# Performance work log

Measured on AMD Instinct MI355X. Metric: run time of the kernel, lower is better.

## Reference

```python
import jax, jax.numpy as jnp
import numpy as np

NUM_HEADS = 16
NUM_KV_HEADS = 4
HEAD_SIZE = 128
SCALE = 1.0 / np.sqrt(128.0).astype(np.float32)
NEG_INF = -1e30


def setup_inputs() -> dict:
    key = jax.random.key(0)
    kq, kk, kv = jax.random.split(key, 3)
    B, S = 2, 2048
    query = jax.random.normal(kq, (B, NUM_HEADS, S, HEAD_SIZE), dtype=jnp.float32)
    k = jax.random.normal(kk, (B, NUM_KV_HEADS, S, HEAD_SIZE), dtype=jnp.float32)
    v = jax.random.normal(kv, (B, NUM_KV_HEADS, S, HEAD_SIZE), dtype=jnp.float32)
    return {"query": query, "key": k, "value": v}


def _attn(query, key, value):
    # query: [B, H, S, D]; key/value: [B, Hkv, S, D]; GQA with group = H // Hkv
    B, H, S, D = query.shape
    Hkv = key.shape[1]
    G = H // Hkv
    q = query.reshape(B, Hkv, G, S, D)
    # scores: [B, Hkv, G, Sq, Sk]
    scores = jnp.einsum('bkgsd,bktd->bkgst', q, key) * jnp.float32(SCALE)
    causal = jnp.tril(jnp.ones((S, S), dtype=bool))  # [Sq, Sk]
    scores = jnp.where(causal, scores, jnp.float32(NEG_INF))
    probs = jax.nn.softmax(scores, axis=-1)
    out = jnp.einsum('bkgst,bktd->bkgsd', probs, value)  # [B, Hkv, G, S, D]
    out = out.reshape(B, H, S, D)
    # transpose(1,2).reshape -> [B, S, H*D]
    return out.transpose(0, 2, 1, 3).reshape(B, S, H * D)


def reference(query, key, value):
    return _attn(query, key, value)
```

## Files before the change

### kernel.cpp

```cpp
#include <hip/hip_runtime.h>


#define S_LEN 2048
#define DH    128
#define NH    16
#define NKVH  4
#define NB    2
#define TQ    128
#define TK    64
#define NQT   (S_LEN / TQ)
#define PROW  72
#define QSCALE 0.12752749610559243f

typedef __attribute__((ext_vector_type(8))) short short8;
typedef __attribute__((ext_vector_type(4))) float f32x4;

#if __has_builtin(__builtin_amdgcn_exp2f)
#define EX2(x) __builtin_amdgcn_exp2f(x)
#else
#define EX2(x) exp2f(x)
#endif

__device__ __forceinline__ unsigned short bf1(float a) {
    union { float f; unsigned u; } x; x.f = a;
    return (unsigned short)((x.u + 0x8000u) >> 16);
}
__device__ __forceinline__ unsigned pk2(float a, float b) {
    union { float f; unsigned u; } x, y; x.f = a; y.f = b;
    return ((x.u + 0x8000u) >> 16) | ((y.u + 0x8000u) & 0xffff0000u);
}
__device__ __forceinline__ void cp16(const void* g, void* lds) {
    __builtin_amdgcn_global_load_lds(
        (const __attribute__((address_space(1))) void*)g,
        (__attribute__((address_space(3))) void*)lds, 16, 0, 0);
}

__global__ __launch_bounds__(256, 4)
void prepack(const float* __restrict__ K, const float* __restrict__ V,
             unsigned short* __restrict__ Kb, unsigned short* __restrict__ Vt) {
    const long long flat = (long long)blockIdx.x * 2048 + threadIdx.x * 8;
    const int s = (int)(flat >> 7) & (S_LEN - 1);
    const int d0 = (int)flat & 127;
    if (blockIdx.y == 0) {
        const float* p = K + flat;
        float4 x = *(const float4*)p;
        float4 y = *(const float4*)(p + 4);
        const int cs = (d0 >> 3) ^ (s & 7);
        uint4 o;
        o.x = pk2(x.x, x.y); o.y = pk2(x.z, x.w);
        o.z = pk2(y.x, y.y); o.w = pk2(y.z, y.w);
        *(uint4*)(Kb + (flat & ~127LL) + cs * 8) = o;
    } else {
        const float* p = V + flat;
        float4 x = *(const float4*)p;
        float4 y = *(const float4*)(p + 4);
        float vals[8] = {x.x, x.y, x.z, x.w, y.x, y.y, y.z, y.w};
        unsigned short* vt = Vt + ((flat >> 18) << 18);
        const int sc = (s >> 3) & 7, sbase = s & ~63, soff = s & 7;
#pragma unroll
        for (int dd = 0; dd < 8; ++dd) {
            const int d = d0 + dd;
            vt[(long long)d * S_LEN + sbase + ((sc ^ (d & 7)) << 3) + soff] = bf1(vals[dd]);
        }
    }
}

__global__ __launch_bounds__(256, 2)
void attn_fwd(const float* __restrict__ Q,
              const unsigned short* __restrict__ Kb,
              const unsigned short* __restrict__ Vtg,
              float* __restrict__ O) {
    const int qt  = NQT - 1 - blockIdx.x;
    const int h   = blockIdx.y;
    const int b   = blockIdx.z;
    const int kvh = h >> 2;

    const int tid  = threadIdx.x;
    const int w    = tid >> 6;
    const int lane = tid & 63;
    const int quad = lane >> 4;
    const int l16  = lane & 15;
    const int swz  = l16 & 7;

    __shared__ alignas(16) unsigned short Kl[TK][DH];
    __shared__ alignas(16) unsigned short Vl[DH][TK];
    __shared__ alignas(16) unsigned short Pl[TQ][PROW];

    const unsigned short* kb = Kb  + ((size_t)b * NKVH + kvh) * (size_t)(S_LEN * DH);
    const unsigned short* vb = Vtg + ((size_t)b * NKVH + kvh) * (size_t)(S_LEN * DH);

    const int wq0 = qt * TQ + w * 32;
    short8 aq[2][4];
#pragma unroll
    for (int sub = 0; sub < 2; ++sub) {
        const float* qp = Q + (((size_t)b * NH + h) * S_LEN + wq0 + sub * 16 + l16) * DH;
#pragma unroll
        for (int dc = 0; dc < 4; ++dc) {
            float4 x = *(const float4*)(qp + dc * 32 + quad * 8);
            float4 y = *(const float4*)(qp + dc * 32 + quad * 8 + 4);
            union { unsigned u[4]; short8 s; } t;
            t.u[0] = pk2(x.x * QSCALE, x.y * QSCALE);
            t.u[1] = pk2(x.z * QSCALE, x.w * QSCALE);
            t.u[2] = pk2(y.x * QSCALE, y.y * QSCALE);
            t.u[3] = pk2(y.z * QSCALE, y.w * QSCALE);
            aq[sub][dc] = t.s;
        }
    }

    f32x4 o[2][8];
#pragma unroll
    for (int sub = 0; sub < 2; ++sub)
#pragma unroll
        for (int ch = 0; ch < 8; ++ch) o[sub][ch] = (f32x4){0.f, 0.f, 0.f, 0.f};
    float lsum[2][4];
#pragma unroll
    for (int sub = 0; sub < 2; ++sub)
#pragma unroll
        for (int r = 0; r < 4; ++r) lsum[sub][r] = 0.f;

    const int nt  = 2 * qt + 2;
    const int ntw = 2 * qt + 1 + (w >> 1);

    for (int t = 0; t < nt; ++t) {
        const int j0 = t * TK;
        __syncthreads();
        {
            const char* ks = (const char*)(kb + (size_t)j0 * DH);
#pragma unroll
            for (int i = 0; i < 4; ++i)
                cp16(ks + w * 4096 + i * 1024 + lane * 16,
                     (char*)&Kl[0][0] + w * 4096 + i * 1024);
            const char* vs = (const char*)vb;
#pragma unroll
            for (int i = 0; i < 4; ++i) {
                const int row  = w * 32 + i * 8 + (lane >> 3);
                const int colB = (lane & 7) * 16;
                cp16(vs + (size_t)row * (S_LEN * 2) + j0 * 2 + colB,
                     (char*)&Vl[0][0] + w * 4096 + i * 1024);
            }
        }
        __syncthreads();

        if (t < ntw) {
            const bool diag = (t == ntw - 1);
            f32x4 s[2][4];
#pragma unroll
            for (int sub = 0; sub < 2; ++sub)
#pragma unroll
                for (int k4 = 0; k4 < 4; ++k4) s[sub][k4] = (f32x4){0.f, 0.f, 0.f, 0.f};
#pragma unroll
            for (int dc = 0; dc < 4; ++dc) {
#pragma unroll
                for (int k4 = 0; k4 < 4; ++k4) {
                    short8 bk = *(const short8*)&Kl[k4 * 16 + l16][((dc * 4 + quad) ^ swz) * 8];
                    s[0][k4] = __builtin_amdgcn_mfma_f32_16x16x32_bf16(aq[0][dc], bk, s[0][k4], 0, 0, 0);
                    s[1][k4] = __builtin_amdgcn_mfma_f32_16x16x32_bf16(aq[1][dc], bk, s[1][k4], 0, 0, 0);
                }
            }
#pragma unroll
            for (int sub = 0; sub < 2; ++sub) {
                const int rb = wq0 + sub * 16 + quad * 4;
#pragma unroll
                for (int r = 0; r < 4; ++r) {
                    float v0 = s[sub][0][r], v1 = s[sub][1][r];
                    float v2 = s[sub][2][r], v3 = s[sub][3][r];
                    if (diag) {
                        const int row = rb + r;
                        if (j0 + l16      > row) v0 = -1e30f;
                        if (j0 + 16 + l16 > row) v1 = -1e30f;
                        if (j0 + 32 + l16 > row) v2 = -1e30f;
                        if (j0 + 48 + l16 > row) v3 = -1e30f;
                    }
                    float p0 = EX2(v0), p1 = EX2(v1), p2 = EX2(v2), p3 = EX2(v3);
                    lsum[sub][r] += (p0 + p1) + (p2 + p3);
                    const int prow = w * 32 + sub * 16 + quad * 4 + r;
                    Pl[prow][l16]      = bf1(p0);
                    Pl[prow][16 + l16] = bf1(p1);
                    Pl[prow][32 + l16] = bf1(p2);
                    Pl[prow][48 + l16] = bf1(p3);
                }
            }
#pragma unroll
            for (int kc = 0; kc < 2; ++kc) {
                short8 ap0 = *(const short8*)&Pl[w * 32 + l16][kc * 32 + quad * 8];
                short8 ap1 = *(const short8*)&Pl[w * 32 + 16 + l16][kc * 32 + quad * 8];
#pragma unroll
                for (int ch = 0; ch < 8; ++ch) {
                    short8 bv = *(const short8*)&Vl[ch * 16 + l16][((kc * 4 + quad) ^ swz) * 8];
                    o[0][ch] = __builtin_amdgcn_mfma_f32_16x16x32_bf16(ap0, bv, o[0][ch], 0, 0, 0);
                    o[1][ch] = __builtin_amdgcn_mfma_f32_16x16x32_bf16(ap1, bv, o[1][ch], 0, 0, 0);
                }
            }
        }
    }

#pragma unroll
    for (int sub = 0; sub < 2; ++sub) {
#pragma unroll
        for (int r = 0; r < 4; ++r) {
            float rs = lsum[sub][r];
            rs += __shfl_xor(rs, 1);
            rs += __shfl_xor(rs, 2);
            rs += __shfl_xor(rs, 4);
            rs += __shfl_xor(rs, 8);
            const float invl = 1.f / rs;
            const int row = wq0 + sub * 16 + quad * 4 + r;
            float* op = O + ((size_t)b * S_LEN + row) * (NH * DH) + h * DH;
#pragma unroll
            for (int ch = 0; ch < 8; ++ch)
                op[ch * 16 + l16] = o[sub][ch][r] * invl;
        }
    }
}

extern "C" void kernel_launch(void* const* d_in, const int* in_sizes, int n_in,
                              void* d_out, int out_size, void* d_ws, size_t ws_size,
                              hipStream_t stream) {
    const float* Q = (const float*)d_in[0];
    const float* K = (const float*)d_in[1];
    const float* V = (const float*)d_in[2];
    float* O = (float*)d_out;
    unsigned short* Kb = (unsigned short*)d_ws;
    unsigned short* Vt = Kb + (size_t)NB * NKVH * S_LEN * DH;
    dim3 pgrid(NB * NKVH * (S_LEN / 16), 2);
    prepack<<<pgrid, 256, 0, stream>>>(K, V, Kb, Vt);
    dim3 grid(NQT, NH, NB);
    attn_fwd<<<grid, 256, 0, stream>>>(Q, Kb, Vt, O);
}
```

Before: 170.9 us.

## Transpose V through LDS in prepack, pack P stores, reorder attention grid

The V prepack now stages a 64x32 tile in shared memory and writes coalesced 16-byte rows of the transposed, swizzled layout, replacing scattered 2-byte global stores. In the attention kernel, P is written to LDS as packed 8-byte stores with a permuted key order that the V layout mirrors. The grid is flattened to 1D with batch 0 scheduled heavy-first and batch 1 light-first, to balance causal work across CUs. The mixed ordering of the two batches risks an uneven tail.

```diff
diff --git a/kernel.cpp b/kernel.cpp
--- a/kernel.cpp
+++ b/kernel.cpp
@@ -38,10 +38,10 @@
 __global__ __launch_bounds__(256, 4)
 void prepack(const float* __restrict__ K, const float* __restrict__ V,
              unsigned short* __restrict__ Kb, unsigned short* __restrict__ Vt) {
-    const long long flat = (long long)blockIdx.x * 2048 + threadIdx.x * 8;
-    const int s = (int)(flat >> 7) & (S_LEN - 1);
-    const int d0 = (int)flat & 127;
     if (blockIdx.y == 0) {
+        const long long flat = (long long)blockIdx.x * 2048 + threadIdx.x * 8;
+        const int s = (int)(flat >> 7) & (S_LEN - 1);
+        const int d0 = (int)flat & 127;
         const float* p = K + flat;
         float4 x = *(const float4*)p;
         float4 y = *(const float4*)(p + 4);
@@ -51,17 +51,37 @@
         o.z = pk2(y.x, y.y); o.w = pk2(y.z, y.w);
         *(uint4*)(Kb + (flat & ~127LL) + cs * 8) = o;
     } else {
-        const float* p = V + flat;
-        float4 x = *(const float4*)p;
-        float4 y = *(const float4*)(p + 4);
-        float vals[8] = {x.x, x.y, x.z, x.w, y.x, y.y, y.z, y.w};
-        unsigned short* vt = Vt + ((flat >> 18) << 18);
-        const int sc = (s >> 3) & 7, sbase = s & ~63, soff = s & 7;
-#pragma unroll
-        for (int dd = 0; dd < 8; ++dd) {
-            const int d = d0 + dd;
-            vt[(long long)d * S_LEN + sbase + ((sc ^ (d & 7)) << 3) + soff] = bf1(vals[dd]);
-        }
+        const int x = blockIdx.x;
+        const int bkvh = x >> 7, sblk = (x >> 2) & 31, q = x & 3;
+        const int tid = threadIdx.x;
+        __shared__ unsigned Lt[64][17];
+        const float* base = V + (size_t)bkvh * S_LEN * DH + (size_t)sblk * 64 * DH + q * 32;
+#pragma unroll
+        for (int j = 0; j < 2; ++j) {
+            const int e = tid + j * 256;
+            const int s = e >> 3, c4 = e & 7;
+            float4 v = *(const float4*)(base + (size_t)s * DH + c4 * 4);
+            Lt[s][c4 * 2]     = pk2(v.x, v.y);
+            Lt[s][c4 * 2 + 1] = pk2(v.z, v.w);
+        }
+        __syncthreads();
+        const unsigned short* lt = (const unsigned short*)&Lt[0][0];
+        const int d_loc = tid >> 3, pc = tid & 7;
+        const int d = q * 32 + d_loc;
+        const int c_log = pc ^ (d & 7);
+        unsigned short vv[8];
+#pragma unroll
+        for (int j = 0; j < 8; ++j) {
+            const int kp = c_log * 8 + j;
+            const int kv = (kp & 3) * 16 + (kp >> 2);
+            vv[j] = lt[kv * 34 + d_loc];
+        }
+        uint4 o;
+        o.x = (unsigned)vv[0] | ((unsigned)vv[1] << 16);
+        o.y = (unsigned)vv[2] | ((unsigned)vv[3] << 16);
+        o.z = (unsigned)vv[4] | ((unsigned)vv[5] << 16);
+        o.w = (unsigned)vv[6] | ((unsigned)vv[7] << 16);
+        *(uint4*)(Vt + (size_t)bkvh * S_LEN * DH + (size_t)d * S_LEN + sblk * 64 + pc * 8) = o;
     }
 }
 
@@ -70,9 +90,11 @@
               const unsigned short* __restrict__ Kb,
               const unsigned short* __restrict__ Vtg,
               float* __restrict__ O) {
-    const int qt  = NQT - 1 - blockIdx.x;
-    const int h   = blockIdx.y;
-    const int b   = blockIdx.z;
+    const int n  = blockIdx.x;
+    const int x  = n & 15;
+    const int h  = (n >> 4) & 15;
+    const int b  = n >> 8;
+    const int qt = b ? x : (NQT - 1 - x);
     const int kvh = h >> 2;
 
     const int tid  = threadIdx.x;
@@ -96,13 +118,13 @@
         const float* qp = Q + (((size_t)b * NH + h) * S_LEN + wq0 + sub * 16 + l16) * DH;
 #pragma unroll
         for (int dc = 0; dc < 4; ++dc) {
-            float4 x = *(const float4*)(qp + dc * 32 + quad * 8);
-            float4 y = *(const float4*)(qp + dc * 32 + quad * 8 + 4);
+            float4 xx = *(const float4*)(qp + dc * 32 + quad * 8);
+            float4 yy = *(const float4*)(qp + dc * 32 + quad * 8 + 4);
             union { unsigned u[4]; short8 s; } t;
-            t.u[0] = pk2(x.x * QSCALE, x.y * QSCALE);
-            t.u[1] = pk2(x.z * QSCALE, x.w * QSCALE);
-            t.u[2] = pk2(y.x * QSCALE, y.y * QSCALE);
-            t.u[3] = pk2(y.z * QSCALE, y.w * QSCALE);
+            t.u[0] = pk2(xx.x * QSCALE, xx.y * QSCALE);
+            t.u[1] = pk2(xx.z * QSCALE, xx.w * QSCALE);
+            t.u[2] = pk2(yy.x * QSCALE, yy.y * QSCALE);
+            t.u[3] = pk2(yy.z * QSCALE, yy.w * QSCALE);
             aq[sub][dc] = t.s;
         }
     }
@@ -174,10 +196,7 @@
                     float p0 = EX2(v0), p1 = EX2(v1), p2 = EX2(v2), p3 = EX2(v3);
                     lsum[sub][r] += (p0 + p1) + (p2 + p3);
                     const int prow = w * 32 + sub * 16 + quad * 4 + r;
-                    Pl[prow][l16]      = bf1(p0);
-                    Pl[prow][16 + l16] = bf1(p1);
-                    Pl[prow][32 + l16] = bf1(p2);
-                    Pl[prow][48 + l16] = bf1(p3);
+                    *(uint2*)&Pl[prow][l16 * 4] = make_uint2(pk2(p0, p1), pk2(p2, p3));
                 }
             }
 #pragma unroll
@@ -224,6 +243,5 @@
     unsigned short* Vt = Kb + (size_t)NB * NKVH * S_LEN * DH;
     dim3 pgrid(NB * NKVH * (S_LEN / 16), 2);
     prepack<<<pgrid, 256, 0, stream>>>(K, V, Kb, Vt);
-    dim3 grid(NQT, NH, NB);
-    attn_fwd<<<grid, 256, 0, stream>>>(Q, Kb, Vt, O);
-}
+    attn_fwd<<<dim3(512), 256, 0, stream>>>(Q, Kb, Vt, O);
+}
```

After: 153.0 us. 10.5% less time.
